# Kernel optimization log

Hardware: AMD Instinct MI355X
Metric: run time of the kernel (lower is better)

The kernel has to match this reference:

```python
import jax, jax.numpy as jnp
import numpy as np

NUM_TAG = 128
T, B = 1024, 512


def setup_inputs() -> dict:
    key = jax.random.key(0)
    k_em, k_tag, k_s, k_t, k_e = jax.random.split(key, 5)
    emissions = jax.random.normal(k_em, (T, B, NUM_TAG), dtype=jnp.float32)
    tags = jax.random.randint(k_tag, (T, B), 0, NUM_TAG, dtype=jnp.int32)
    mask = jnp.ones((T, B), dtype=jnp.float32)
    # parameters: uniform(-0.1, 0.1) as in reset_params
    start_transitions = jax.random.uniform(k_s, (NUM_TAG,), minval=-0.1, maxval=0.1, dtype=jnp.float32)
    transitions = jax.random.uniform(k_t, (NUM_TAG, NUM_TAG), minval=-0.1, maxval=0.1, dtype=jnp.float32)
    end_transitions = jax.random.uniform(k_e, (NUM_TAG,), minval=-0.1, maxval=0.1, dtype=jnp.float32)
    return {
        "emissions": emissions,
        "tags": tags,
        "mask": mask,
        "start_transitions": start_transitions,
        "transitions": transitions,
        "end_transitions": end_transitions,
    }


def _path_score(emissions, tags, mask, start_transitions, transitions, end_transitions):
    # emissions: [T,B,K], tags/mask: [T,B]
    b_idx = jnp.arange(tags.shape[1])
    # emission score of the gold tag at each step: [T,B]
    em_tag = jnp.take_along_axis(emissions, tags[:, :, None].astype(jnp.int32), axis=2)[:, :, 0]
    scores = start_transitions[tags[0]] + (em_tag * mask).sum(axis=0)
    # transition scores along the gold path, masked: [T-1,B]
    scores = scores + (transitions[tags[:-1], tags[1:]] * mask[1:]).sum(axis=0)
    last_idx = mask.astype(jnp.int32).sum(axis=0) - 1  # [B]
    last_tag = tags[last_idx, b_idx]
    return scores + end_transitions[last_tag]


def _log_partition(emissions, mask, start_transitions, transitions, end_transitions):
    log_prob0 = start_transitions[None, :] + emissions[0]  # [B,K]

    def step(log_prob, xs):
        em_t, m_t = xs  # [B,K], [B]
        # score[b,i,j] = log_prob[b,i] + transitions[i,j] + em_t[b,j]
        score = jax.nn.logsumexp(
            log_prob[:, :, None] + transitions[None, :, :] + em_t[:, None, :], axis=1
        )
        new_lp = score * m_t[:, None] + log_prob * (1.0 - m_t)[:, None]
        return new_lp, None

    log_prob, _ = jax.lax.scan(step, log_prob0, (emissions[1:], mask[1:]))
    return jax.nn.logsumexp(log_prob + end_transitions[None, :], axis=1)  # [B]


def reference(emissions, tags, mask, start_transitions, transitions, end_transitions):
    path = _path_score(emissions, tags, mask, start_transitions, transitions, end_transitions)
    log_z = _log_partition(emissions, mask, start_transitions, transitions, end_transitions)
    return (path - log_z).sum()
```

## Files before the change

kernel.cpp:

```cpp
#include <hip/hip_runtime.h>
#include <cstdint>

#define TT 1024
#define BB 512
#define KK 128
#define ST 136

typedef __attribute__((ext_vector_type(8))) short short8;
typedef __attribute__((ext_vector_type(4))) float f4;

__device__ __forceinline__ unsigned short f2bf_rtne(float x) {
  unsigned u = __float_as_uint(x);
  u += 0x7FFF + ((u >> 16) & 1);
  return (unsigned short)(u >> 16);
}

__device__ __forceinline__ unsigned pack_trunc(float l, float h) {
  return __builtin_amdgcn_perm(__float_as_uint(h), __float_as_uint(l), 0x07060302u);
}

__device__ __forceinline__ void lgkm_barrier() {
  __atomic_signal_fence(__ATOMIC_SEQ_CST);
  __builtin_amdgcn_s_waitcnt(0xC07F);
  __builtin_amdgcn_s_barrier();
  __atomic_signal_fence(__ATOMIC_SEQ_CST);
}

__global__ __launch_bounds__(256, 1) void crf_forward(
    const float* __restrict__ em, const float* __restrict__ mask,
    const float* __restrict__ start_t, const float* __restrict__ trans,
    const float* __restrict__ end_t, float* __restrict__ logz)
{
  const int tid  = threadIdx.x;
  const int w    = __builtin_amdgcn_readfirstlane(tid >> 6);
  const int lane = tid & 63;
  const int q    = lane >> 4;
  const int lo   = lane & 15;
  const int b0   = blockIdx.x * 16;

  __shared__ __align__(16) unsigned short Pt[2][16 * ST];
  __shared__ __align__(16) float mxs[16][4];
  __shared__ __align__(16) float psm[16][4];

  const int cb0 = 32 * w + 4 * q;
  const int cb1 = cb0 + 16;

  const size_t TS = (size_t)BB * KK;
  const float* emrow = em + (size_t)(b0 + lo) * KK;

  short8 Af[2][4];
#pragma unroll
  for (int mti = 0; mti < 2; ++mti) {
    const int col = 16 * (2 * w + mti) + lo;
#pragma unroll
    for (int kt = 0; kt < 4; ++kt) {
      short8 v;
#pragma unroll
      for (int j = 0; j < 8; ++j) {
        const int k = 32 * kt + 8 * q + j;
        v[j] = (short)f2bf_rtne(__expf(trans[(size_t)k * KK + col]));
      }
      Af[mti][kt] = v;
    }
  }

  f4 S0, S1;
  float base = 0.f;
  {
    const f4 e0a = *(const f4*)(emrow + cb0);
    const f4 e0b = *(const f4*)(emrow + cb1);
    const f4 st0 = *(const f4*)(start_t + cb0);
    const f4 st1 = *(const f4*)(start_t + cb1);
#pragma unroll
    for (int i = 0; i < 4; ++i) {
      S0[i] = __expf(st0[i] + e0a[i]);
      S1[i] = __expf(st1[i] + e0b[i]);
    }
    *(uint2*)&Pt[0][lo * ST + cb0] =
        make_uint2(pack_trunc(S0[0], S0[1]), pack_trunc(S0[2], S0[3]));
    *(uint2*)&Pt[0][lo * ST + cb1] =
        make_uint2(pack_trunc(S1[0], S1[1]), pack_trunc(S1[2], S1[3]));
  }

  f4 eaC = *(const f4*)(emrow + 1 * TS + cb0);
  f4 ebC = *(const f4*)(emrow + 1 * TS + cb1);
  f4 eaN = *(const f4*)(emrow + 2 * TS + cb0);
  f4 ebN = *(const f4*)(emrow + 2 * TS + cb1);
  float mkC = mask[1 * BB + b0 + lo];
  float mkN = mask[2 * BB + b0 + lo];

  for (int t = 1; t < TT; ++t) {
    const int pb = (t & 1) ^ 1;

    lgkm_barrier();

    float ps = 1.0f, kln2 = 0.f;
    const bool scale_step = ((t & 3) == 1) && (t > 1);
    if (scale_step) {
      const f4 mv4 = *(const f4*)&mxs[lo][0];
      const float mv = fmaxf(fmaxf(mv4[0], mv4[1]), fmaxf(mv4[2], mv4[3]));
      const int k = (int)(__float_as_uint(mv) >> 23) - 127;
      ps = __uint_as_float((unsigned)(127 - k) << 23);
      kln2 = (float)k * 0.6931471805599453f;
    }

    short8 Bf[4];
#pragma unroll
    for (int kt = 0; kt < 4; ++kt)
      Bf[kt] = *(const short8*)&Pt[pb][lo * ST + 32 * kt + 8 * q];

    const int tp = (t + 2 < TT) ? (t + 2) : (TT - 1);
    const f4 eaL = *(const f4*)(emrow + (size_t)tp * TS + cb0);
    const f4 ebL = *(const f4*)(emrow + (size_t)tp * TS + cb1);
    const float mkL = mask[tp * BB + b0 + lo];

    f4 X0, X1;
#pragma unroll
    for (int i = 0; i < 4; ++i) { X0[i] = __expf(eaC[i]); X1[i] = __expf(ebC[i]); }
    if (scale_step) { X0 *= ps; X1 *= ps; }

    f4 a0 = {0.f, 0.f, 0.f, 0.f}, a1 = {0.f, 0.f, 0.f, 0.f};
#pragma unroll
    for (int kt = 0; kt < 4; ++kt) {
      a0 = __builtin_amdgcn_mfma_f32_16x16x32_bf16(Af[0][kt], Bf[kt], a0, 0, 0, 0);
      a1 = __builtin_amdgcn_mfma_f32_16x16x32_bf16(Af[1][kt], Bf[kt], a1, 0, 0, 0);
    }

    const bool upd = (mkC != 0.f);
#pragma unroll
    for (int i = 0; i < 4; ++i) {
      const float n0 = a0[i] * X0[i];
      const float n1 = a1[i] * X1[i];
      S0[i] = upd ? n0 : S0[i];
      S1[i] = upd ? n1 : S1[i];
    }
    if (scale_step && upd) base += kln2;

    *(uint2*)&Pt[t & 1][lo * ST + cb0] =
        make_uint2(pack_trunc(S0[0], S0[1]), pack_trunc(S0[2], S0[3]));
    *(uint2*)&Pt[t & 1][lo * ST + cb1] =
        make_uint2(pack_trunc(S1[0], S1[1]), pack_trunc(S1[2], S1[3]));

    if ((t & 3) == 0) {
      float mv = fmaxf(fmaxf(fmaxf(S0[0], S0[1]), fmaxf(S0[2], S0[3])),
                       fmaxf(fmaxf(S1[0], S1[1]), fmaxf(S1[2], S1[3])));
      mv = fmaxf(mv, __shfl_xor(mv, 16));
      mv = fmaxf(mv, __shfl_xor(mv, 32));
      if (q == 0) mxs[lo][w] = mv;
    }

    eaC = eaN; ebC = ebN; eaN = eaL; ebN = ebL;
    mkC = mkN; mkN = mkL;
  }

  {
    const f4 ed0 = *(const f4*)(end_t + cb0);
    const f4 ed1 = *(const f4*)(end_t + cb1);
    float s = 0.f;
#pragma unroll
    for (int i = 0; i < 4; ++i)
      s += S0[i] * __expf(ed0[i]) + S1[i] * __expf(ed1[i]);
    s += __shfl_xor(s, 16);
    s += __shfl_xor(s, 32);
    if (q == 0) psm[lo][w] = s;
    __syncthreads();
    if (tid < 16) {
      const f4 pv = *(const f4*)&psm[tid][0];
      logz[b0 + tid] = base + logf(pv[0] + pv[1] + pv[2] + pv[3]);
    }
  }
}

__global__ __launch_bounds__(512) void crf_path_tb(
    const float* __restrict__ em, const int* __restrict__ tags,
    const float* __restrict__ mask, const float* __restrict__ trans,
    float* __restrict__ ws_tb)
{
  const int t = blockIdx.x, b = threadIdx.x;
  const int tg = tags[t * BB + b];
  const float mk = mask[t * BB + b];
  float v = em[((size_t)t * BB + b) * KK + tg] * mk;
  if (t >= 1) {
    const int tgp = tags[(t - 1) * BB + b];
    v += trans[(size_t)tgp * KK + tg] * mk;
  }
  __shared__ float red[8];
#pragma unroll
  for (int off = 32; off; off >>= 1) v += __shfl_xor(v, off);
  if ((b & 63) == 0) red[b >> 6] = v;
  __syncthreads();
  if (b == 0) {
    float s = 0.f;
#pragma unroll
    for (int i = 0; i < 8; ++i) s += red[i];
    ws_tb[t] = s;
  }
}

__global__ __launch_bounds__(64) void crf_bterm(
    const int* __restrict__ tags, const float* __restrict__ mask,
    const float* __restrict__ start_t, const float* __restrict__ end_t,
    float* __restrict__ ws_bt)
{
  const int b = blockIdx.x, tid = threadIdx.x;
  float ms = 0.f;
  for (int t = tid; t < TT; t += 64) ms += mask[t * BB + b];
#pragma unroll
  for (int off = 32; off; off >>= 1) ms += __shfl_xor(ms, off);
  if (tid == 0) {
    const int last = (int)(ms + 0.5f) - 1;
    ws_bt[b] = start_t[tags[b]] + end_t[tags[(size_t)last * BB + b]];
  }
}

__global__ __launch_bounds__(1024) void crf_final(
    const float* __restrict__ ws_tb, const float* __restrict__ ws_bt,
    const float* __restrict__ ws_lz, float* __restrict__ out)
{
  const int tid = threadIdx.x;
  float v = ws_tb[tid];
  if (tid < BB) v += ws_bt[tid] - ws_lz[tid];
  __shared__ float red[16];
#pragma unroll
  for (int off = 32; off; off >>= 1) v += __shfl_xor(v, off);
  if ((tid & 63) == 0) red[tid >> 6] = v;
  __syncthreads();
  if (tid == 0) {
    float s = 0.f;
#pragma unroll
    for (int i = 0; i < 16; ++i) s += red[i];
    out[0] = s;
  }
}

extern "C" void kernel_launch(void* const* d_in, const int* in_sizes, int n_in,
                              void* d_out, int out_size, void* d_ws, size_t ws_size,
                              hipStream_t stream) {
  (void)in_sizes; (void)n_in; (void)out_size; (void)ws_size;
  const float* em    = (const float*)d_in[0];
  const int*   tags  = (const int*)  d_in[1];
  const float* mask  = (const float*)d_in[2];
  const float* st    = (const float*)d_in[3];
  const float* trans = (const float*)d_in[4];
  const float* et    = (const float*)d_in[5];
  float* out = (float*)d_out;

  float* ws_tb = (float*)d_ws;
  float* ws_bt = ws_tb + 1024;
  float* ws_lz = ws_bt + 512;

  crf_path_tb<<<TT, 512, 0, stream>>>(em, tags, mask, trans, ws_tb);
  crf_bterm  <<<BB, 64, 0, stream>>>(tags, mask, st, et, ws_bt);
  crf_forward<<<32, 256, 0, stream>>>(em, mask, st, trans, et, ws_lz);
  crf_final  <<<1, 1024, 0, stream>>>(ws_tb, ws_bt, ws_lz, out);
}
```

Measured before the change: 1.109 ms.

## Run forward recursion in a single wavefront with register-resident state

The forward CRF recursion now runs each 16-sequence tile on one 64-lane wavefront instead of four. That one wave holds all 8 column tiles of exp(transitions) and the full state in registers. The B operand for the next step is repacked directly from the MFMA output layout by permuting the K index, which removes the LDS round trip and the per-step block barrier. The step loop is also unrolled by two with ping-pong emission prefetch buffers. The cost is four times more MFMA and exp work serialized per wave and higher register pressure, with still only 32 wavefronts on the whole GPU.

```diff
diff --git a/kernel.cpp b/kernel.cpp
--- a/kernel.cpp
+++ b/kernel.cpp
@@ -4,10 +4,10 @@
 #define TT 1024
 #define BB 512
 #define KK 128
-#define ST 136
 
 typedef __attribute__((ext_vector_type(8))) short short8;
 typedef __attribute__((ext_vector_type(4))) float f4;
+typedef __attribute__((ext_vector_type(4))) unsigned int uint4v;
 
 __device__ __forceinline__ unsigned short f2bf_rtne(float x) {
   unsigned u = __float_as_uint(x);
@@ -19,155 +19,148 @@
   return __builtin_amdgcn_perm(__float_as_uint(h), __float_as_uint(l), 0x07060302u);
 }
 
-__device__ __forceinline__ void lgkm_barrier() {
-  __atomic_signal_fence(__ATOMIC_SEQ_CST);
-  __builtin_amdgcn_s_waitcnt(0xC07F);
-  __builtin_amdgcn_s_barrier();
-  __atomic_signal_fence(__ATOMIC_SEQ_CST);
-}
-
-__global__ __launch_bounds__(256, 1) void crf_forward(
+__global__ __launch_bounds__(64, 1) void crf_forward(
     const float* __restrict__ em, const float* __restrict__ mask,
     const float* __restrict__ start_t, const float* __restrict__ trans,
     const float* __restrict__ end_t, float* __restrict__ logz)
 {
-  const int tid  = threadIdx.x;
-  const int w    = __builtin_amdgcn_readfirstlane(tid >> 6);
-  const int lane = tid & 63;
+  const int lane = threadIdx.x & 63;
   const int q    = lane >> 4;
   const int lo   = lane & 15;
   const int b0   = blockIdx.x * 16;
 
-  __shared__ __align__(16) unsigned short Pt[2][16 * ST];
-  __shared__ __align__(16) float mxs[16][4];
-  __shared__ __align__(16) float psm[16][4];
-
-  const int cb0 = 32 * w + 4 * q;
-  const int cb1 = cb0 + 16;
-
   const size_t TS = (size_t)BB * KK;
-  const float* emrow = em + (size_t)(b0 + lo) * KK;
-
-  short8 Af[2][4];
-#pragma unroll
-  for (int mti = 0; mti < 2; ++mti) {
-    const int col = 16 * (2 * w + mti) + lo;
+  const float* emlane = em + (size_t)(b0 + lo) * KK + 4 * q;
+  const float* mrow   = mask + (b0 + lo);
+
+  short8 Af[8][4];
+#pragma unroll
+  for (int mt = 0; mt < 8; ++mt)
 #pragma unroll
     for (int kt = 0; kt < 4; ++kt) {
       short8 v;
 #pragma unroll
       for (int j = 0; j < 8; ++j) {
-        const int k = 32 * kt + 8 * q + j;
-        v[j] = (short)f2bf_rtne(__expf(trans[(size_t)k * KK + col]));
+        const int ck = 32 * kt + 16 * (j >> 2) + 4 * q + (j & 3);
+        v[j] = (short)f2bf_rtne(__expf(trans[(size_t)ck * KK + 16 * mt + lo]));
       }
-      Af[mti][kt] = v;
-    }
-  }
-
-  f4 S0, S1;
-  float base = 0.f;
-  {
-    const f4 e0a = *(const f4*)(emrow + cb0);
-    const f4 e0b = *(const f4*)(emrow + cb1);
-    const f4 st0 = *(const f4*)(start_t + cb0);
-    const f4 st1 = *(const f4*)(start_t + cb1);
-#pragma unroll
-    for (int i = 0; i < 4; ++i) {
-      S0[i] = __expf(st0[i] + e0a[i]);
-      S1[i] = __expf(st1[i] + e0b[i]);
-    }
-    *(uint2*)&Pt[0][lo * ST + cb0] =
-        make_uint2(pack_trunc(S0[0], S0[1]), pack_trunc(S0[2], S0[3]));
-    *(uint2*)&Pt[0][lo * ST + cb1] =
-        make_uint2(pack_trunc(S1[0], S1[1]), pack_trunc(S1[2], S1[3]));
-  }
-
-  f4 eaC = *(const f4*)(emrow + 1 * TS + cb0);
-  f4 ebC = *(const f4*)(emrow + 1 * TS + cb1);
-  f4 eaN = *(const f4*)(emrow + 2 * TS + cb0);
-  f4 ebN = *(const f4*)(emrow + 2 * TS + cb1);
-  float mkC = mask[1 * BB + b0 + lo];
-  float mkN = mask[2 * BB + b0 + lo];
-
-  for (int t = 1; t < TT; ++t) {
-    const int pb = (t & 1) ^ 1;
-
-    lgkm_barrier();
-
+      Af[mt][kt] = v;
+    }
+
+  f4 S[8];
+  uint4v PB[4];
+  float base = 0.f, mvPrev = 1.0f;
+#pragma unroll
+  for (int mt = 0; mt < 8; ++mt) {
+    const f4 e0 = *(const f4*)(emlane + 16 * mt);
+    const f4 st = *(const f4*)(start_t + 16 * mt + 4 * q);
+#pragma unroll
+    for (int i = 0; i < 4; ++i) S[mt][i] = __expf(st[i] + e0[i]);
+  }
+#pragma unroll
+  for (int kt = 0; kt < 4; ++kt) {
+    PB[kt][0] = pack_trunc(S[2 * kt][0],     S[2 * kt][1]);
+    PB[kt][1] = pack_trunc(S[2 * kt][2],     S[2 * kt][3]);
+    PB[kt][2] = pack_trunc(S[2 * kt + 1][0], S[2 * kt + 1][1]);
+    PB[kt][3] = pack_trunc(S[2 * kt + 1][2], S[2 * kt + 1][3]);
+  }
+
+  f4 bufA[8], bufB[8];
+  float mkA, mkB;
+#pragma unroll
+  for (int mt = 0; mt < 8; ++mt) {
+    bufB[mt] = *(const f4*)(emlane + 1 * TS + 16 * mt);
+    bufA[mt] = *(const f4*)(emlane + 2 * TS + 16 * mt);
+  }
+  mkB = mrow[1 * BB];
+  mkA = mrow[2 * BB];
+
+  auto STEP = [&](const int t, f4 (&bufC)[8], float& mkC) {
+    const float mk = mkC;
     float ps = 1.0f, kln2 = 0.f;
     const bool scale_step = ((t & 3) == 1) && (t > 1);
     if (scale_step) {
-      const f4 mv4 = *(const f4*)&mxs[lo][0];
-      const float mv = fmaxf(fmaxf(mv4[0], mv4[1]), fmaxf(mv4[2], mv4[3]));
-      const int k = (int)(__float_as_uint(mv) >> 23) - 127;
+      const int k = (int)(__float_as_uint(mvPrev) >> 23) - 127;
       ps = __uint_as_float((unsigned)(127 - k) << 23);
       kln2 = (float)k * 0.6931471805599453f;
     }
 
+    f4 X[8];
+#pragma unroll
+    for (int mt = 0; mt < 8; ++mt) {
+      f4 x;
+#pragma unroll
+      for (int i = 0; i < 4; ++i) x[i] = __expf(bufC[mt][i]);
+      if (scale_step) x *= ps;
+      X[mt] = x;
+    }
+
+    const int tp = (t + 2 < TT) ? (t + 2) : (TT - 1);
+    const float* p = emlane + (size_t)tp * TS;
+#pragma unroll
+    for (int mt = 0; mt < 8; ++mt) bufC[mt] = *(const f4*)(p + 16 * mt);
+    mkC = mrow[(size_t)tp * BB];
+
     short8 Bf[4];
 #pragma unroll
+    for (int kt = 0; kt < 4; ++kt) Bf[kt] = __builtin_bit_cast(short8, PB[kt]);
+
+    f4 acc[8];
+#pragma unroll
+    for (int mt = 0; mt < 8; ++mt) acc[mt] = f4{0.f, 0.f, 0.f, 0.f};
+#pragma unroll
     for (int kt = 0; kt < 4; ++kt)
-      Bf[kt] = *(const short8*)&Pt[pb][lo * ST + 32 * kt + 8 * q];
-
-    const int tp = (t + 2 < TT) ? (t + 2) : (TT - 1);
-    const f4 eaL = *(const f4*)(emrow + (size_t)tp * TS + cb0);
-    const f4 ebL = *(const f4*)(emrow + (size_t)tp * TS + cb1);
-    const float mkL = mask[tp * BB + b0 + lo];
-
-    f4 X0, X1;
-#pragma unroll
-    for (int i = 0; i < 4; ++i) { X0[i] = __expf(eaC[i]); X1[i] = __expf(ebC[i]); }
-    if (scale_step) { X0 *= ps; X1 *= ps; }
-
-    f4 a0 = {0.f, 0.f, 0.f, 0.f}, a1 = {0.f, 0.f, 0.f, 0.f};
+#pragma unroll
+      for (int mt = 0; mt < 8; ++mt)
+        acc[mt] = __builtin_amdgcn_mfma_f32_16x16x32_bf16(Af[mt][kt], Bf[kt], acc[mt], 0, 0, 0);
+
+    const bool upd = (mk != 0.f);
+#pragma unroll
+    for (int mt = 0; mt < 8; ++mt)
+#pragma unroll
+      for (int i = 0; i < 4; ++i) {
+        const float n = acc[mt][i] * X[mt][i];
+        S[mt][i] = upd ? n : S[mt][i];
+      }
+    if (scale_step && upd) base += kln2;
+
 #pragma unroll
     for (int kt = 0; kt < 4; ++kt) {
-      a0 = __builtin_amdgcn_mfma_f32_16x16x32_bf16(Af[0][kt], Bf[kt], a0, 0, 0, 0);
-      a1 = __builtin_amdgcn_mfma_f32_16x16x32_bf16(Af[1][kt], Bf[kt], a1, 0, 0, 0);
-    }
-
-    const bool upd = (mkC != 0.f);
-#pragma unroll
-    for (int i = 0; i < 4; ++i) {
-      const float n0 = a0[i] * X0[i];
-      const float n1 = a1[i] * X1[i];
-      S0[i] = upd ? n0 : S0[i];
-      S1[i] = upd ? n1 : S1[i];
-    }
-    if (scale_step && upd) base += kln2;
-
-    *(uint2*)&Pt[t & 1][lo * ST + cb0] =
-        make_uint2(pack_trunc(S0[0], S0[1]), pack_trunc(S0[2], S0[3]));
-    *(uint2*)&Pt[t & 1][lo * ST + cb1] =
-        make_uint2(pack_trunc(S1[0], S1[1]), pack_trunc(S1[2], S1[3]));
+      PB[kt][0] = pack_trunc(S[2 * kt][0],     S[2 * kt][1]);
+      PB[kt][1] = pack_trunc(S[2 * kt][2],     S[2 * kt][3]);
+      PB[kt][2] = pack_trunc(S[2 * kt + 1][0], S[2 * kt + 1][1]);
+      PB[kt][3] = pack_trunc(S[2 * kt + 1][2], S[2 * kt + 1][3]);
+    }
 
     if ((t & 3) == 0) {
-      float mv = fmaxf(fmaxf(fmaxf(S0[0], S0[1]), fmaxf(S0[2], S0[3])),
-                       fmaxf(fmaxf(S1[0], S1[1]), fmaxf(S1[2], S1[3])));
+      float mv = S[0][0];
+#pragma unroll
+      for (int mt = 0; mt < 8; ++mt)
+#pragma unroll
+        for (int i = 0; i < 4; ++i) mv = fmaxf(mv, S[mt][i]);
       mv = fmaxf(mv, __shfl_xor(mv, 16));
       mv = fmaxf(mv, __shfl_xor(mv, 32));
-      if (q == 0) mxs[lo][w] = mv;
-    }
-
-    eaC = eaN; ebC = ebN; eaN = eaL; ebN = ebL;
-    mkC = mkN; mkN = mkL;
-  }
+      mvPrev = mv;
+    }
+  };
+
+  for (int t = 1; t + 1 < TT; t += 2) {
+    STEP(t, bufB, mkB);
+    STEP(t + 1, bufA, mkA);
+  }
+  STEP(TT - 1, bufB, mkB);
 
   {
-    const f4 ed0 = *(const f4*)(end_t + cb0);
-    const f4 ed1 = *(const f4*)(end_t + cb1);
     float s = 0.f;
 #pragma unroll
-    for (int i = 0; i < 4; ++i)
-      s += S0[i] * __expf(ed0[i]) + S1[i] * __expf(ed1[i]);
+    for (int mt = 0; mt < 8; ++mt) {
+      const f4 ed = *(const f4*)(end_t + 16 * mt + 4 * q);
+#pragma unroll
+      for (int i = 0; i < 4; ++i) s += S[mt][i] * __expf(ed[i]);
+    }
     s += __shfl_xor(s, 16);
     s += __shfl_xor(s, 32);
-    if (q == 0) psm[lo][w] = s;
-    __syncthreads();
-    if (tid < 16) {
-      const f4 pv = *(const f4*)&psm[tid][0];
-      logz[b0 + tid] = base + logf(pv[0] + pv[1] + pv[2] + pv[3]);
-    }
+    if (q == 0) logz[b0 + lo] = base + logf(s);
   }
 }
 
@@ -251,6 +244,6 @@
 
   crf_path_tb<<<TT, 512, 0, stream>>>(em, tags, mask, trans, ws_tb);
   crf_bterm  <<<BB, 64, 0, stream>>>(tags, mask, st, et, ws_bt);
-  crf_forward<<<32, 256, 0, stream>>>(em, mask, st, trans, et, ws_lz);
+  crf_forward<<<32, 64, 0, stream>>>(em, mask, st, trans, et, ws_lz);
   crf_final  <<<1, 1024, 0, stream>>>(ws_tb, ws_bt, ws_lz, out);
 }
```

New measurement: 1.236 ms. +11.4%, slower.
